# Kernel optimization log

Measured on AMD Instinct MI355X. Metric: run time of the kernel, lower is better.

## Reference

```python
import jax, jax.numpy as jnp
import numpy as np

NUM_EXPERTS = 16
EFF_THRESHOLD = 0.1
SIM_THRESHOLD = 0.0
EPS = 1e-8


def setup_inputs() -> dict:
    key = jax.random.key(0)
    k1, k2 = jax.random.split(key)
    B, E, H = 4096, NUM_EXPERTS, 1024
    rp = jax.random.uniform(k1, (B, E), dtype=jnp.float32)
    rp = rp / rp.sum(axis=-1, keepdims=True)  # valid probabilities
    emb = jax.random.normal(k2, (B, H), dtype=jnp.float32)
    return {"routing_probs": rp, "input_embeddings": emb}


def _total_loss(routing_probs, input_embeddings):
    B, E = routing_probs.shape

    # --- LoadBalanceLoss: var(mean usage) / (1/E)^2, unbiased var (torch default)
    usage = routing_probs.mean(axis=0)                      # [E]
    var = jnp.sum((usage - usage.mean()) ** 2) / (E - 1)
    load_balance = var * (E ** 2)

    # --- EntropyRegularizationLoss (target None): -mean entropy
    entropy = -jnp.sum(routing_probs * jnp.log(routing_probs + EPS), axis=-1)
    entropy_loss = -entropy.mean()

    # --- EfficiencyLoss: sum of probs below threshold, averaged over batch
    small = jnp.where(routing_probs < EFF_THRESHOLD, routing_probs, 0.0)
    efficiency = small.sum(axis=-1).mean()

    # --- ConsistencyLoss: mean KL(softmax(p_j) || softmax(p_i)) over similar pairs
    logp = jax.nn.log_softmax(routing_probs, axis=-1)       # [B, E]
    q = jnp.exp(logp)                                       # [B, E]
    neg_ent_q = jnp.sum(q * logp, axis=-1)                  # [B], = sum q log q
    # KL[i, j] = sum_e q_j (log q_j - logp_i) = neg_ent_q[j] - logp_i . q_j
    kl = neg_ent_q[None, :] - jnp.einsum('ie,je->ij', logp, q)  # [B, B]

    nemb = input_embeddings / jnp.linalg.norm(input_embeddings, axis=-1, keepdims=True)
    sim = nemb @ nemb.T                                     # [B, B]
    mask = (sim > SIM_THRESHOLD) & (~jnp.eye(B, dtype=bool))
    num_pairs = mask.sum()
    cons_sum = jnp.sum(jnp.where(mask, kl, 0.0))
    consistency = jnp.where(num_pairs > 0,
                            cons_sum / jnp.maximum(num_pairs, 1).astype(kl.dtype),
                            0.0)

    return load_balance + entropy_loss + efficiency + consistency


def reference(routing_probs, input_embeddings):
    return _total_loss(routing_probs, input_embeddings)
```

## Files before the change

kernel.cpp:

```cpp
#include <hip/hip_runtime.h>
#include <hip/hip_bf16.h>

#define BROWS 4096
#define NE    16
#define HDIM  1024
#define ACC_F 128
#define NTILE 32
#define NBLK  (NTILE * (NTILE + 1) / 2)

typedef __attribute__((ext_vector_type(8))) short short8;
typedef __attribute__((ext_vector_type(4))) float float4v;

__device__ __forceinline__ unsigned bf16rne(float f) {
    const unsigned u = __float_as_uint(f);
    return (u + 0x7FFFu + ((u >> 16) & 1u)) >> 16;
}
__device__ __forceinline__ unsigned pk2(float lo, float hi) {
    return bf16rne(lo) | (bf16rne(hi) << 16);
}

__device__ __forceinline__ void row16f(const float* src, float* p) {
    const float4v* pv = (const float4v*)src;
    float4v a0 = pv[0], a1 = pv[1], a2 = pv[2], a3 = pv[3];
    p[0]=a0.x; p[1]=a0.y; p[2]=a0.z; p[3]=a0.w;
    p[4]=a1.x; p[5]=a1.y; p[6]=a1.z; p[7]=a1.w;
    p[8]=a2.x; p[9]=a2.y; p[10]=a2.z; p[11]=a2.w;
    p[12]=a3.x; p[13]=a3.y; p[14]=a3.z; p[15]=a3.w;
}

__device__ __forceinline__ void lsm16(const float* p, float* lp, float* q, float& ne) {
    float m = p[0];
#pragma unroll
    for (int e = 1; e < 16; e++) m = fmaxf(m, p[e]);
    float s = 0.f;
#pragma unroll
    for (int e = 0; e < 16; e++) s += expf(p[e] - m);
    const float ls = logf(s);
    ne = 0.f;
#pragma unroll
    for (int e = 0; e < 16; e++) {
        lp[e] = p[e] - m - ls;
        q[e]  = expf(lp[e]);
        ne   += q[e] * lp[e];
    }
}

__global__ __launch_bounds__(256) void conv_init(
    const float* __restrict__ src, unsigned short* __restrict__ dst, float* __restrict__ acc)
{
    if (blockIdx.x == 0 && threadIdx.x < ACC_F) acc[threadIdx.x] = 0.f;
    const size_t i = ((size_t)blockIdx.x * 256 + threadIdx.x) * 8;
    float4v a = *(const float4v*)(src + i);
    float4v b = *(const float4v*)(src + i + 4);
    uint4 w = {pk2(a.x,a.y), pk2(a.z,a.w), pk2(b.x,b.y), pk2(b.z,b.w)};
    *(uint4*)(dst + i) = w;
}

__device__ __forceinline__ void decode_pair(int id, int& bi, int& bj) {
    int L = (id & 7) * 66 + (id >> 3);
    int gi = 0, gj = 0;
    for (;;) {
        const int cnt = (gi == gj) ? 10 : 16;
        if (L < cnt) break;
        L -= cnt;
        gj++; if (gj == 8) { gi++; gj = gi; }
    }
    if (gi == gj) {
        int u = 0, c = 4;
        while (L >= c) { L -= c; u++; c--; }
        bi = gi * 4 + u; bj = gj * 4 + u + L;
    } else {
        bi = gi * 4 + (L >> 2); bj = gj * 4 + (L & 3);
    }
}

template<bool PRE>
__global__ __launch_bounds__(512, 4) void gram_kl(
    const float* __restrict__ embf, const unsigned short* __restrict__ embb,
    const float* __restrict__ rp, float* __restrict__ acc,
    unsigned int* __restrict__ out)
{
    __shared__ char smem[32768];
    __shared__ float red[16];
    __shared__ int islast;
    __shared__ float fin[96];
    __hip_bfloat16* tA = (__hip_bfloat16*)smem;
    __hip_bfloat16* tB = (__hip_bfloat16*)(smem + 8192);
    __hip_bfloat16* eAF = (__hip_bfloat16*)smem;
    __hip_bfloat16* eBF = (__hip_bfloat16*)(smem + 8192);
    __hip_bfloat16* eAR = (__hip_bfloat16*)(smem + 16384);
    __hip_bfloat16* eBR = (__hip_bfloat16*)(smem + 24576);

    int bi, bj;
    decode_pair((int)blockIdx.x, bi, bj);

    const int t = threadIdx.x;
    const int lane = t & 63, wid = t >> 6;
    const int wi0 = (wid >> 1) * 32, wj0 = (wid & 1) * 64;
    const int lrow = lane & 15, quad = lane >> 4;

    const int row = t >> 2, cp = t & 3;
    const int sw  = cp ^ ((row >> 1) & 3);
    const int off = row * 32 + sw * 8;

    float4v accf[2][4];
#pragma unroll
    for (int a = 0; a < 2; a++)
#pragma unroll
        for (int b = 0; b < 4; b++) { accf[a][b].x=0.f; accf[a][b].y=0.f; accf[a][b].z=0.f; accf[a][b].w=0.f; }

    int roA[2], roB[4];
#pragma unroll
    for (int f = 0; f < 2; f++) {
        const int ra = wi0 + f * 16 + lrow;
        roA[f] = ra * 32 + (quad ^ ((ra >> 1) & 3)) * 8;
    }
#pragma unroll
    for (int f = 0; f < 4; f++) {
        const int rb = wj0 + f * 16 + lrow;
        roB[f] = rb * 32 + (quad ^ ((rb >> 1) & 3)) * 8;
    }

    if (PRE) {
        const unsigned short* gA = embb + (size_t)(bi * 128) * HDIM + (size_t)row * HDIM + cp * 8;
        const unsigned short* gB = embb + (size_t)(bj * 128) * HDIM + (size_t)row * HDIM + cp * 8;
        uint4 va0 = *(const uint4*)(gA);
        uint4 vb0 = *(const uint4*)(gB);
        uint4 va1 = *(const uint4*)(gA + 32);
        uint4 vb1 = *(const uint4*)(gB + 32);
        for (int kt = 0; kt < HDIM; kt += 64) {
            __syncthreads();
            *(uint4*)(tA + off) = va0;
            *(uint4*)(tB + off) = vb0;
            __syncthreads();
            {
                const int kn = (kt + 64 < HDIM) ? (kt + 64) : kt;
                va0 = *(const uint4*)(gA + kn);
                vb0 = *(const uint4*)(gB + kn);
            }
            {
                short8 a[2], b[4];
#pragma unroll
                for (int f = 0; f < 2; f++) a[f] = *(const short8*)(tA + roA[f]);
#pragma unroll
                for (int f = 0; f < 4; f++) b[f] = *(const short8*)(tB + roB[f]);
#pragma unroll
                for (int fi = 0; fi < 2; fi++)
#pragma unroll
                    for (int fj = 0; fj < 4; fj++)
                        accf[fi][fj] = __builtin_amdgcn_mfma_f32_16x16x32_bf16(
                            a[fi], b[fj], accf[fi][fj], 0, 0, 0);
            }
            __syncthreads();
            *(uint4*)(tA + off) = va1;
            *(uint4*)(tB + off) = vb1;
            __syncthreads();
            {
                const int kn = (kt + 96 < HDIM) ? (kt + 96) : (kt + 32);
                va1 = *(const uint4*)(gA + kn);
                vb1 = *(const uint4*)(gB + kn);
            }
            {
                short8 a[2], b[4];
#pragma unroll
                for (int f = 0; f < 2; f++) a[f] = *(const short8*)(tA + roA[f]);
#pragma unroll
                for (int f = 0; f < 4; f++) b[f] = *(const short8*)(tB + roB[f]);
#pragma unroll
                for (int fi = 0; fi < 2; fi++)
#pragma unroll
                    for (int fj = 0; fj < 4; fj++)
                        accf[fi][fj] = __builtin_amdgcn_mfma_f32_16x16x32_bf16(
                            a[fi], b[fj], accf[fi][fj], 0, 0, 0);
            }
        }
    } else {
        const float* gA = embf + (size_t)(bi * 128) * HDIM;
        const float* gB = embf + (size_t)(bj * 128) * HDIM;
        float4v a0, a1, b0, b1;
        {
            const float* pa = gA + (size_t)row * HDIM + cp * 8;
            const float* pb = gB + (size_t)row * HDIM + cp * 8;
            a0 = *(const float4v*)pa; a1 = *(const float4v*)(pa + 4);
            b0 = *(const float4v*)pb; b1 = *(const float4v*)(pb + 4);
        }
        for (int kt = 0; kt < HDIM; kt += 32) {
            uint4 wa = {pk2(a0.x,a0.y), pk2(a0.z,a0.w), pk2(a1.x,a1.y), pk2(a1.z,a1.w)};
            uint4 wb = {pk2(b0.x,b0.y), pk2(b0.z,b0.w), pk2(b1.x,b1.y), pk2(b1.z,b1.w)};
            __syncthreads();
            *(uint4*)(tA + off) = wa;
            *(uint4*)(tB + off) = wb;
            __syncthreads();
            const int kn = (kt + 32 < HDIM) ? (kt + 32) : kt;
            const float* pa = gA + (size_t)row * HDIM + kn + cp * 8;
            const float* pb = gB + (size_t)row * HDIM + kn + cp * 8;
            a0 = *(const float4v*)pa; a1 = *(const float4v*)(pa + 4);
            b0 = *(const float4v*)pb; b1 = *(const float4v*)(pb + 4);
            short8 a[2], b[4];
#pragma unroll
            for (int f = 0; f < 2; f++) a[f] = *(const short8*)(tA + roA[f]);
#pragma unroll
            for (int f = 0; f < 4; f++) b[f] = *(const short8*)(tB + roB[f]);
#pragma unroll
            for (int fi = 0; fi < 2; fi++)
#pragma unroll
                for (int fj = 0; fj < 4; fj++)
                    accf[fi][fj] = __builtin_amdgcn_mfma_f32_16x16x32_bf16(
                        a[fi], b[fj], accf[fi][fj], 0, 0, 0);
        }
    }
    __syncthreads();

    {
        float p[16], lp[16], q[16], ne;
        const bool iSide = (t < 128);
        if (t < 256) {
            const int rloc = iSide ? t : (t - 128);
            const int grow = (iSide ? bi : bj) * 128 + rloc;
            row16f(rp + (size_t)grow * NE, p);
            lsm16(p, lp, q, ne);
            float r1[16], r2[16], x1, x2;
            if (iSide) {
#pragma unroll
                for (int e = 0; e < 16; e++) { r1[e] = lp[e]; r2[e] = q[e]; }
                x1 = 1.f; x2 = ne;
            } else {
#pragma unroll
                for (int e = 0; e < 16; e++) { r1[e] = -q[e]; r2[e] = -lp[e]; }
                x1 = ne; x2 = 1.f;
            }
            const int s = (rloc >> 1) & 3;
            __hip_bfloat16* d1 = (iSide ? eAF : eBF) + rloc * 32;
            __hip_bfloat16* d2 = (iSide ? eAR : eBR) + rloc * 32;
            uint4 w0 = {pk2(r1[0],r1[1]), pk2(r1[2],r1[3]), pk2(r1[4],r1[5]), pk2(r1[6],r1[7])};
            uint4 w1 = {pk2(r1[8],r1[9]), pk2(r1[10],r1[11]), pk2(r1[12],r1[13]), pk2(r1[14],r1[15])};
            uint4 w2 = {pk2(x1, 0.f), 0u, 0u, 0u};
            uint4 w3 = {0u, 0u, 0u, 0u};
            *(uint4*)(d1 + (0 ^ s) * 8) = w0;
            *(uint4*)(d1 + (1 ^ s) * 8) = w1;
            *(uint4*)(d1 + (2 ^ s) * 8) = w2;
            *(uint4*)(d1 + (3 ^ s) * 8) = w3;
            uint4 v0 = {pk2(r2[0],r2[1]), pk2(r2[2],r2[3]), pk2(r2[4],r2[5]), pk2(r2[6],r2[7])};
            uint4 v1 = {pk2(r2[8],r2[9]), pk2(r2[10],r2[11]), pk2(r2[12],r2[13]), pk2(r2[14],r2[15])};
            uint4 v2 = {pk2(x2, 0.f), 0u, 0u, 0u};
            *(uint4*)(d2 + (0 ^ s) * 8) = v0;
            *(uint4*)(d2 + (1 ^ s) * 8) = v1;
            *(uint4*)(d2 + (2 ^ s) * 8) = v2;
            *(uint4*)(d2 + (3 ^ s) * 8) = w3;
        }
        if (bi == bj && iSide) {
            float ent = 0.f, eff = 0.f;
#pragma unroll
            for (int e = 0; e < 16; e++) {
                ent += p[e] * logf(p[e] + 1e-8f);
                if (p[e] < 0.1f) eff += p[e];
            }
#pragma unroll
            for (int e = 0; e < 18; e++) {
                float v = (e < 16) ? p[e] : ((e == 16) ? ent : eff);
#pragma unroll
                for (int off2 = 32; off2 > 0; off2 >>= 1) v += __shfl_down(v, off2);
                if (lane == 0) atomicAdd(&acc[e], v);
            }
        }
    }
    __syncthreads();

    float4v accF[2][4], accR[2][4];
    {
        const float4v z = {0.f, 0.f, 0.f, 0.f};
        short8 af[2], ar[2], bfr[4], brr[4];
#pragma unroll
        for (int f = 0; f < 2; f++) {
            af[f] = *(const short8*)(eAF + roA[f]);
            ar[f] = *(const short8*)(eAR + roA[f]);
        }
#pragma unroll
        for (int f = 0; f < 4; f++) {
            bfr[f] = *(const short8*)(eBF + roB[f]);
            brr[f] = *(const short8*)(eBR + roB[f]);
        }
#pragma unroll
        for (int fi = 0; fi < 2; fi++)
#pragma unroll
            for (int fj = 0; fj < 4; fj++) {
                accF[fi][fj] = __builtin_amdgcn_mfma_f32_16x16x32_bf16(af[fi], bfr[fj], z, 0, 0, 0);
                accR[fi][fj] = __builtin_amdgcn_mfma_f32_16x16x32_bf16(ar[fi], brr[fj], z, 0, 0, 0);
            }
    }

    float klacc = 0.f, cntacc = 0.f;
    const bool offd = (bi != bj);
#pragma unroll
    for (int fi = 0; fi < 2; fi++) {
#pragma unroll
        for (int fj = 0; fj < 4; fj++) {
#pragma unroll
            for (int rg = 0; rg < 4; rg++) {
                const int ig = bi * 128 + wi0 + fi * 16 + quad * 4 + rg;
                const int jg = bj * 128 + wj0 + fj * 16 + lrow;
                const float g = accf[fi][fj][rg];
                if ((g > 0.f) && (ig != jg)) {
                    klacc  += accF[fi][fj][rg];
                    cntacc += 1.f;
                    if (offd) { klacc += accR[fi][fj][rg]; cntacc += 1.f; }
                }
            }
        }
    }

#pragma unroll
    for (int off2 = 32; off2 > 0; off2 >>= 1) {
        klacc  += __shfl_down(klacc, off2);
        cntacc += __shfl_down(cntacc, off2);
    }
    if (lane == 0) { red[wid] = klacc; red[8 + wid] = cntacc; }
    __syncthreads();
    if (t == 0) {
        float k = 0.f, c = 0.f;
#pragma unroll
        for (int w = 0; w < 8; w++) { k += red[w]; c += red[8 + w]; }
        atomicAdd(&acc[18 + ((int)blockIdx.x & 31)], k);
        atomicAdd(&acc[50 + ((int)blockIdx.x & 31)], c);
        const unsigned got = __hip_atomic_fetch_add((unsigned int*)(acc + 82), 1u,
                                                    __ATOMIC_RELEASE, __HIP_MEMORY_SCOPE_AGENT);
        islast = (got == NBLK - 1) ? 1 : 0;
    }
    __syncthreads();

    if (islast) {
        if (t == 0)
            (void)__hip_atomic_load((unsigned int*)(acc + 82), __ATOMIC_ACQUIRE,
                                    __HIP_MEMORY_SCOPE_AGENT);
        __syncthreads();
        if (t < 82)
            fin[t] = __hip_atomic_load(&acc[t], __ATOMIC_RELAXED, __HIP_MEMORY_SCOPE_AGENT);
        __syncthreads();
        if (t == 0) {
            float u[16], usum = 0.f;
#pragma unroll
            for (int e = 0; e < 16; e++) { u[e] = fin[e] / (float)BROWS; usum += u[e]; }
            const float mean = usum / 16.f;
            float var = 0.f;
#pragma unroll
            for (int e = 0; e < 16; e++) { float dd = u[e] - mean; var += dd * dd; }
            var /= 15.f;
            const float lb  = var * 256.f;
            const float ent = fin[16] / (float)BROWS;
            const float eff = fin[17] / (float)BROWS;
            float kl = 0.f, cnt = 0.f;
#pragma unroll
            for (int s = 0; s < 32; s++) { kl += fin[18 + s]; cnt += fin[50 + s]; }
            const float cons = (cnt > 0.f) ? (kl / fmaxf(cnt, 1.f)) : 0.f;
            const float total = lb + ent + eff + cons;
            const unsigned fb   = __float_as_uint(total);
            const unsigned hi   = fb >> 16;
            const unsigned mant = fb & 0xFFFFu;
            const unsigned rnd  = (mant > 0x8000u || (mant == 0x8000u && (hi & 1))) ? 1u : 0u;
            out[0] = (fb & 0xFFFF0000u) | ((hi + rnd) & 0xFFFFu);
        }
    }
}

extern "C" void kernel_launch(void* const* d_in, const int* in_sizes, int n_in,
                              void* d_out, int out_size, void* d_ws, size_t ws_size,
                              hipStream_t stream) {
    const float* rp  = (const float*)d_in[0];
    const float* emb = (const float*)d_in[1];
    float* acc = (float*)d_ws;
    unsigned short* embb = (unsigned short*)((char*)d_ws + ACC_F * sizeof(float));
    (void)in_sizes; (void)n_in; (void)out_size;

    const size_t need = ACC_F * sizeof(float) + (size_t)BROWS * HDIM * 2;
    const bool pre = (ws_size >= need);

    if (pre) {
        conv_init<<<(BROWS * HDIM) / (256 * 8), 256, 0, stream>>>(emb, embb, acc);
        gram_kl<true><<<NBLK, 512, 0, stream>>>(emb, embb, rp, acc, (unsigned int*)d_out);
    } else {
        conv_init<<<1, 256, 0, stream>>>(emb, embb, acc);
        gram_kl<false><<<NBLK, 512, 0, stream>>>(emb, (const unsigned short*)nullptr, rp, acc,
                                                 (unsigned int*)d_out);
    }
}
```

Before: 117.9 us.

## Double-buffer 64-wide K tiles in LDS with one barrier per step

The Gram-matrix main loop now stages 64-element K slices for both 128-row tiles into two alternating 32KB LDS buffers with an 8-way XOR swizzle. Each iteration needs only a single __syncthreads instead of two per 32-wide step, and it issues 16 MFMAs per barrier. The aim is to cut barrier and LDS round-trip overhead and expose more overlap between global prefetch and MFMA work. The cost is LDS usage rising from 32KB to 64KB per block, which may lower occupancy under launch_bounds(512,4), and the fp32 path loses its register prefetch.

```diff
diff --git a/kernel.cpp b/kernel.cpp
--- a/kernel.cpp
+++ b/kernel.cpp
@@ -80,12 +80,10 @@
     const float* __restrict__ rp, float* __restrict__ acc,
     unsigned int* __restrict__ out)
 {
-    __shared__ char smem[32768];
+    __shared__ char smem[65536];
     __shared__ float red[16];
     __shared__ int islast;
     __shared__ float fin[96];
-    __hip_bfloat16* tA = (__hip_bfloat16*)smem;
-    __hip_bfloat16* tB = (__hip_bfloat16*)(smem + 8192);
     __hip_bfloat16* eAF = (__hip_bfloat16*)smem;
     __hip_bfloat16* eBF = (__hip_bfloat16*)(smem + 8192);
     __hip_bfloat16* eAR = (__hip_bfloat16*)(smem + 16384);
@@ -99,9 +97,25 @@
     const int wi0 = (wid >> 1) * 32, wj0 = (wid & 1) * 64;
     const int lrow = lane & 15, quad = lane >> 4;
 
-    const int row = t >> 2, cp = t & 3;
-    const int sw  = cp ^ ((row >> 1) & 3);
-    const int off = row * 32 + sw * 8;
+    const int srow = t >> 3, spos = t & 7;
+    const int so0 = srow * 64 + (spos ^ (srow & 7)) * 8;
+    const int so1 = so0 + 64 * 64;
+
+    int koA[2][2], koB[4][2];
+#pragma unroll
+    for (int f = 0; f < 2; f++) {
+        const int r = wi0 + f * 16 + lrow;
+#pragma unroll
+        for (int s = 0; s < 2; s++)
+            koA[f][s] = r * 64 + ((s * 4 + quad) ^ (r & 7)) * 8;
+    }
+#pragma unroll
+    for (int f = 0; f < 4; f++) {
+        const int r = wj0 + f * 16 + lrow;
+#pragma unroll
+        for (int s = 0; s < 2; s++)
+            koB[f][s] = r * 64 + ((s * 4 + quad) ^ (r & 7)) * 8;
+    }
 
     float4v accf[2][4];
 #pragma unroll
@@ -109,104 +123,81 @@
 #pragma unroll
         for (int b = 0; b < 4; b++) { accf[a][b].x=0.f; accf[a][b].y=0.f; accf[a][b].z=0.f; accf[a][b].w=0.f; }
 
-    int roA[2], roB[4];
-#pragma unroll
-    for (int f = 0; f < 2; f++) {
-        const int ra = wi0 + f * 16 + lrow;
-        roA[f] = ra * 32 + (quad ^ ((ra >> 1) & 3)) * 8;
-    }
-#pragma unroll
-    for (int f = 0; f < 4; f++) {
-        const int rb = wj0 + f * 16 + lrow;
-        roB[f] = rb * 32 + (quad ^ ((rb >> 1) & 3)) * 8;
-    }
-
     if (PRE) {
-        const unsigned short* gA = embb + (size_t)(bi * 128) * HDIM + (size_t)row * HDIM + cp * 8;
-        const unsigned short* gB = embb + (size_t)(bj * 128) * HDIM + (size_t)row * HDIM + cp * 8;
-        uint4 va0 = *(const uint4*)(gA);
-        uint4 vb0 = *(const uint4*)(gB);
-        uint4 va1 = *(const uint4*)(gA + 32);
-        uint4 vb1 = *(const uint4*)(gB + 32);
-        for (int kt = 0; kt < HDIM; kt += 64) {
+        const unsigned short* gA0 = embb + (size_t)(bi * 128 + srow) * HDIM + spos * 8;
+        const unsigned short* gA1 = gA0 + (size_t)64 * HDIM;
+        const unsigned short* gB0 = embb + (size_t)(bj * 128 + srow) * HDIM + spos * 8;
+        const unsigned short* gB1 = gB0 + (size_t)64 * HDIM;
+        uint4 va0 = *(const uint4*)(gA0), va1 = *(const uint4*)(gA1);
+        uint4 vb0 = *(const uint4*)(gB0), vb1 = *(const uint4*)(gB1);
+        for (int T = 0; T < 16; ++T) {
+            __hip_bfloat16* bufA = (__hip_bfloat16*)(smem + (T & 1) * 32768);
+            __hip_bfloat16* bufB = bufA + 16384 / 2;
+            *(uint4*)(bufA + so0) = va0;
+            *(uint4*)(bufA + so1) = va1;
+            *(uint4*)(bufB + so0) = vb0;
+            *(uint4*)(bufB + so1) = vb1;
+            const int kn = ((T + 1 < 16) ? (T + 1) : T) * 64;
+            va0 = *(const uint4*)(gA0 + kn); va1 = *(const uint4*)(gA1 + kn);
+            vb0 = *(const uint4*)(gB0 + kn); vb1 = *(const uint4*)(gB1 + kn);
             __syncthreads();
-            *(uint4*)(tA + off) = va0;
-            *(uint4*)(tB + off) = vb0;
-            __syncthreads();
-            {
-                const int kn = (kt + 64 < HDIM) ? (kt + 64) : kt;
-                va0 = *(const uint4*)(gA + kn);
-                vb0 = *(const uint4*)(gB + kn);
-            }
-            {
-                short8 a[2], b[4];
-#pragma unroll
-                for (int f = 0; f < 2; f++) a[f] = *(const short8*)(tA + roA[f]);
-#pragma unroll
-                for (int f = 0; f < 4; f++) b[f] = *(const short8*)(tB + roB[f]);
+            short8 a[2][2], b[4][2];
+#pragma unroll
+            for (int f = 0; f < 2; f++)
+#pragma unroll
+                for (int s = 0; s < 2; s++) a[f][s] = *(const short8*)(bufA + koA[f][s]);
+#pragma unroll
+            for (int f = 0; f < 4; f++)
+#pragma unroll
+                for (int s = 0; s < 2; s++) b[f][s] = *(const short8*)(bufB + koB[f][s]);
+#pragma unroll
+            for (int s = 0; s < 2; s++)
 #pragma unroll
                 for (int fi = 0; fi < 2; fi++)
 #pragma unroll
                     for (int fj = 0; fj < 4; fj++)
                         accf[fi][fj] = __builtin_amdgcn_mfma_f32_16x16x32_bf16(
-                            a[fi], b[fj], accf[fi][fj], 0, 0, 0);
-            }
+                            a[fi][s], b[fj][s], accf[fi][fj], 0, 0, 0);
+        }
+    } else {
+        const float* gA0 = embf + (size_t)(bi * 128 + srow) * HDIM + spos * 8;
+        const float* gA1 = gA0 + (size_t)64 * HDIM;
+        const float* gB0 = embf + (size_t)(bj * 128 + srow) * HDIM + spos * 8;
+        const float* gB1 = gB0 + (size_t)64 * HDIM;
+        for (int T = 0; T < 16; ++T) {
+            const int kt = T * 64;
+            __hip_bfloat16* bufA = (__hip_bfloat16*)(smem + (T & 1) * 32768);
+            __hip_bfloat16* bufB = bufA + 16384 / 2;
+            float4v x0 = *(const float4v*)(gA0 + kt), x1 = *(const float4v*)(gA0 + kt + 4);
+            float4v y0 = *(const float4v*)(gA1 + kt), y1 = *(const float4v*)(gA1 + kt + 4);
+            float4v u0 = *(const float4v*)(gB0 + kt), u1 = *(const float4v*)(gB0 + kt + 4);
+            float4v v0 = *(const float4v*)(gB1 + kt), v1 = *(const float4v*)(gB1 + kt + 4);
+            uint4 wa0 = {pk2(x0.x,x0.y), pk2(x0.z,x0.w), pk2(x1.x,x1.y), pk2(x1.z,x1.w)};
+            uint4 wa1 = {pk2(y0.x,y0.y), pk2(y0.z,y0.w), pk2(y1.x,y1.y), pk2(y1.z,y1.w)};
+            uint4 wb0 = {pk2(u0.x,u0.y), pk2(u0.z,u0.w), pk2(u1.x,u1.y), pk2(u1.z,u1.w)};
+            uint4 wb1 = {pk2(v0.x,v0.y), pk2(v0.z,v0.w), pk2(v1.x,v1.y), pk2(v1.z,v1.w)};
+            *(uint4*)(bufA + so0) = wa0;
+            *(uint4*)(bufA + so1) = wa1;
+            *(uint4*)(bufB + so0) = wb0;
+            *(uint4*)(bufB + so1) = wb1;
             __syncthreads();
-            *(uint4*)(tA + off) = va1;
-            *(uint4*)(tB + off) = vb1;
-            __syncthreads();
-            {
-                const int kn = (kt + 96 < HDIM) ? (kt + 96) : (kt + 32);
-                va1 = *(const uint4*)(gA + kn);
-                vb1 = *(const uint4*)(gB + kn);
-            }
-            {
-                short8 a[2], b[4];
-#pragma unroll
-                for (int f = 0; f < 2; f++) a[f] = *(const short8*)(tA + roA[f]);
-#pragma unroll
-                for (int f = 0; f < 4; f++) b[f] = *(const short8*)(tB + roB[f]);
+            short8 a[2][2], b[4][2];
+#pragma unroll
+            for (int f = 0; f < 2; f++)
+#pragma unroll
+                for (int s = 0; s < 2; s++) a[f][s] = *(const short8*)(bufA + koA[f][s]);
+#pragma unroll
+            for (int f = 0; f < 4; f++)
+#pragma unroll
+                for (int s = 0; s < 2; s++) b[f][s] = *(const short8*)(bufB + koB[f][s]);
+#pragma unroll
+            for (int s = 0; s < 2; s++)
 #pragma unroll
                 for (int fi = 0; fi < 2; fi++)
 #pragma unroll
                     for (int fj = 0; fj < 4; fj++)
                         accf[fi][fj] = __builtin_amdgcn_mfma_f32_16x16x32_bf16(
-                            a[fi], b[fj], accf[fi][fj], 0, 0, 0);
-            }
-        }
-    } else {
-        const float* gA = embf + (size_t)(bi * 128) * HDIM;
-        const float* gB = embf + (size_t)(bj * 128) * HDIM;
-        float4v a0, a1, b0, b1;
-        {
-            const float* pa = gA + (size_t)row * HDIM + cp * 8;
-            const float* pb = gB + (size_t)row * HDIM + cp * 8;
-            a0 = *(const float4v*)pa; a1 = *(const float4v*)(pa + 4);
-            b0 = *(const float4v*)pb; b1 = *(const float4v*)(pb + 4);
-        }
-        for (int kt = 0; kt < HDIM; kt += 32) {
-            uint4 wa = {pk2(a0.x,a0.y), pk2(a0.z,a0.w), pk2(a1.x,a1.y), pk2(a1.z,a1.w)};
-            uint4 wb = {pk2(b0.x,b0.y), pk2(b0.z,b0.w), pk2(b1.x,b1.y), pk2(b1.z,b1.w)};
-            __syncthreads();
-            *(uint4*)(tA + off) = wa;
-            *(uint4*)(tB + off) = wb;
-            __syncthreads();
-            const int kn = (kt + 32 < HDIM) ? (kt + 32) : kt;
-            const float* pa = gA + (size_t)row * HDIM + kn + cp * 8;
-            const float* pb = gB + (size_t)row * HDIM + kn + cp * 8;
-            a0 = *(const float4v*)pa; a1 = *(const float4v*)(pa + 4);
-            b0 = *(const float4v*)pb; b1 = *(const float4v*)(pb + 4);
-            short8 a[2], b[4];
-#pragma unroll
-            for (int f = 0; f < 2; f++) a[f] = *(const short8*)(tA + roA[f]);
-#pragma unroll
-            for (int f = 0; f < 4; f++) b[f] = *(const short8*)(tB + roB[f]);
-#pragma unroll
-            for (int fi = 0; fi < 2; fi++)
-#pragma unroll
-                for (int fj = 0; fj < 4; fj++)
-                    accf[fi][fj] = __builtin_amdgcn_mfma_f32_16x16x32_bf16(
-                        a[fi], b[fj], accf[fi][fj], 0, 0, 0);
+                            a[fi][s], b[fj][s], accf[fi][fj], 0, 0, 0);
         }
     }
     __syncthreads();
@@ -259,12 +250,24 @@
             for (int e = 0; e < 18; e++) {
                 float v = (e < 16) ? p[e] : ((e == 16) ? ent : eff);
 #pragma unroll
-                for (int off2 = 32; off2 > 0; off2 >>= 1) v += __shfl_down(v, off2);
+                for (int o = 32; o > 0; o >>= 1) v += __shfl_down(v, o);
                 if (lane == 0) atomicAdd(&acc[e], v);
             }
         }
     }
     __syncthreads();
+
+    int eoA[2], eoB[4];
+#pragma unroll
+    for (int f = 0; f < 2; f++) {
+        const int r = wi0 + f * 16 + lrow;
+        eoA[f] = r * 32 + (quad ^ ((r >> 1) & 3)) * 8;
+    }
+#pragma unroll
+    for (int f = 0; f < 4; f++) {
+        const int r = wj0 + f * 16 + lrow;
+        eoB[f] = r * 32 + (quad ^ ((r >> 1) & 3)) * 8;
+    }
 
     float4v accF[2][4], accR[2][4];
     {
@@ -272,13 +275,13 @@
         short8 af[2], ar[2], bfr[4], brr[4];
 #pragma unroll
         for (int f = 0; f < 2; f++) {
-            af[f] = *(const short8*)(eAF + roA[f]);
-            ar[f] = *(const short8*)(eAR + roA[f]);
+            af[f] = *(const short8*)(eAF + eoA[f]);
+            ar[f] = *(const short8*)(eAR + eoA[f]);
         }
 #pragma unroll
         for (int f = 0; f < 4; f++) {
-            bfr[f] = *(const short8*)(eBF + roB[f]);
-            brr[f] = *(const short8*)(eBR + roB[f]);
+            bfr[f] = *(const short8*)(eBF + eoB[f]);
+            brr[f] = *(const short8*)(eBR + eoB[f]);
         }
 #pragma unroll
         for (int fi = 0; fi < 2; fi++)
@@ -310,9 +313,9 @@
     }
 
 #pragma unroll
-    for (int off2 = 32; off2 > 0; off2 >>= 1) {
-        klacc  += __shfl_down(klacc, off2);
-        cntacc += __shfl_down(cntacc, off2);
+    for (int o = 32; o > 0; o >>= 1) {
+        klacc  += __shfl_down(klacc, o);
+        cntacc += __shfl_down(cntacc, o);
     }
     if (lane == 0) { red[wid] = klacc; red[8 + wid] = cntacc; }
     __syncthreads();
```

Result: faster. 115.4 us (-2.2%).
